# Performance work log

Measured on AMD Instinct MI355X. Metric: run time of the kernel, lower is better.

The kernel has to match this reference:

```python
import jax, jax.numpy as jnp
import numpy as np

B, T, W, H = 4, 4096, 1024, 8
BW = W // H  # block width


@jax.custom_vjp
def sqrt_bound(x):
    return jnp.sqrt(x)

def _sb_fwd(x):
    return jnp.sqrt(x), x

def _sb_bwd(x, g):
    return (g / jnp.sqrt(jnp.clip(4.0 * x, 1e-6)),)

sqrt_bound.defvjp(_sb_fwd, _sb_bwd)


def block_diag_linear(x, w, b):
    # x: [B,T,W] -> [B,T,H,BW]; w: [H,BW,BW]; b: [H,BW]
    xb = x.reshape(x.shape[0], x.shape[1], H, BW)
    y = jnp.einsum('bthi,hij->bthj', xb, w) + b
    return y.reshape(x.shape)


def setup_inputs() -> dict:
    key = jax.random.key(0)
    k1, k2, k3, k4 = jax.random.split(key, 4)
    x = jax.random.normal(k1, (B, T, W), dtype=jnp.float32)
    segment_pos = jnp.broadcast_to(jnp.arange(T, dtype=jnp.int32)[None, :], (B, T))
    std = 1.0 / np.sqrt(BW)
    w_in = std * jax.random.normal(k2, (H, BW, BW), dtype=jnp.float32)
    b_in = jnp.zeros((H, BW), dtype=jnp.float32)
    w_a = std * jax.random.normal(k3, (H, BW, BW), dtype=jnp.float32)
    b_a = jnp.zeros((H, BW), dtype=jnp.float32)
    # rnn_param_init: a_param = log(u^{-0.5} - 1), u ~ U(min_rad^2+eps, max_rad^2+eps)
    u = jax.random.uniform(k4, (W,), dtype=jnp.float32,
                           minval=0.9 ** 2 + 1e-8, maxval=0.999 ** 2 + 1e-8)
    a_param = jnp.log(jnp.exp(-0.5 * jnp.log(u)) - 1.0)
    return {'x': x, 'segment_pos': segment_pos, 'a_param': a_param,
            'w_in': w_in, 'b_in': b_in, 'w_a': w_a, 'b_a': b_a}


def reference(x, segment_pos, a_param, w_in, b_in, w_a, b_a):
    gate_x = jax.nn.sigmoid(block_diag_linear(x, w_in, b_in))
    gate_a = jax.nn.sigmoid(block_diag_linear(x, w_a, b_a))
    log_a = -8.0 * gate_a * jax.nn.softplus(a_param)  # [B,T,W]
    a = jnp.exp(log_a)
    multiplier = sqrt_bound(1.0 - jnp.exp(2.0 * log_a))
    normed_x = x * gate_x * multiplier
    reset = (segment_pos == 0)  # [B,T] bool
    a_eff = a * (~reset)[..., None].astype(a.dtype)
    # diagonal linear recurrence h_t = a_t * h_{t-1} + x_t via lax.scan over time
    def step(h, inp):
        a_t, x_t = inp
        h = a_t * h + x_t
        return h, h
    xs = (jnp.swapaxes(a_eff, 0, 1), jnp.swapaxes(normed_x, 0, 1))  # [T,B,W]
    h0 = jnp.zeros((x.shape[0], x.shape[2]), dtype=x.dtype)
    _, ys = jax.lax.scan(step, h0, xs)
    return jnp.swapaxes(ys, 0, 1)  # [B,T,W]
```

## Files before the change

### kernel.cpp

```cpp
#include <hip/hip_runtime.h>
#include <math.h>

#define NB 4
#define NT 4096
#define NW 1024
#define NH 8
#define CHUNK 64
#define NCH 64
#define STRIDE_A 136

typedef __attribute__((ext_vector_type(8))) short short8;
typedef __attribute__((ext_vector_type(4))) float f32x4;
typedef unsigned long long u64;

__device__ __forceinline__ short bf16rne(float f) {
    unsigned u = __float_as_uint(f);
    u += 0x7fffu + ((u >> 16) & 1u);
    return (short)(u >> 16);
}

__global__ __launch_bounds__(256)
void k0_wfrag(const float* __restrict__ w_in, const float* __restrict__ w_a,
              short* __restrict__ wfH, uint4* __restrict__ poison)
{
    int idx = blockIdx.x * 256 + threadIdx.x;
    uint4 nv; nv.x = nv.y = nv.z = nv.w = 0xFFFFFFFFu;
    poison[idx]         = nv;
    poison[idx + 65536] = nv;

    int j4 = (idx & 31) * 4;
    int i  = (idx >> 5) & 127;
    int h  = (idx >> 12) & 7;
    int g  = idx >> 15;
    const float* w = g ? w_a : w_in;
    float4 v = *(const float4*)&w[((size_t)h * 128 + i) * 128 + j4];
    const float vf[4] = {v.x, v.y, v.z, v.w};
    const int ks = i >> 5, q = (i >> 3) & 3, jj = i & 7;
    #pragma unroll
    for (int d = 0; d < 4; ++d) {
        int j = j4 + d;
        int lane = q * 16 + (j & 15);
        int ntg = j >> 4;
        size_t dst = ((size_t)(((h * 2 + g) * 4 + ks) * 8 + ntg) * 64 + lane) * 8 + jj;
        wfH[dst] = bf16rne(vf[d]);
    }
}

__global__ __launch_bounds__(512)
void k_fused(const float* __restrict__ x, const int* __restrict__ seg,
             const float* __restrict__ a_param,
             const float* __restrict__ b_in, const float* __restrict__ b_a,
             const short* __restrict__ wfH,
             float2* __restrict__ AGH, float* __restrict__ out)
{
    __shared__ short sA[CHUNK * STRIDE_A];
    __shared__ int   sSeg[CHUNK];

    const int h   = blockIdx.x;
    const int bc  = blockIdx.y;
    const int b   = bc >> 6, c = bc & 63;
    const int tid = threadIdx.x;
    const int wave = tid >> 6, lane = tid & 63;
    const int quad = lane >> 4, m = lane & 15;
    const int row0 = b * NT + c * CHUNK;

    {
        const int r  = tid >> 3;
        const int k0 = (tid & 7) * 16;
        const float4* px = (const float4*)(x + (size_t)(row0 + r) * NW + h * 128 + k0);
        float4 v0 = px[0], v1 = px[1], v2 = px[2], v3 = px[3];
        const float f[16] = {v0.x, v0.y, v0.z, v0.w, v1.x, v1.y, v1.z, v1.w,
                             v2.x, v2.y, v2.z, v2.w, v3.x, v3.y, v3.z, v3.w};
        short8 s0, s1;
        #pragma unroll
        for (int j = 0; j < 8; ++j) { s0[j] = bf16rne(f[j]); s1[j] = bf16rne(f[8 + j]); }
        *(short8*)&sA[r * STRIDE_A + k0]     = s0;
        *(short8*)&sA[r * STRIDE_A + k0 + 8] = s1;
        if ((tid & 7) == 0) sSeg[r] = seg[row0 + r];
    }
    __syncthreads();

    f32x4 acc[2][4];
    #pragma unroll
    for (int g = 0; g < 2; ++g)
        #pragma unroll
        for (int mt = 0; mt < 4; ++mt)
            acc[g][mt] = (f32x4){0.f, 0.f, 0.f, 0.f};

    #pragma unroll
    for (int ks = 0; ks < 4; ++ks) {
        short8 ah[4];
        #pragma unroll
        for (int mt = 0; mt < 4; ++mt)
            ah[mt] = *(const short8*)&sA[(mt * 16 + m) * STRIDE_A + ks * 32 + quad * 8];
        #pragma unroll
        for (int g = 0; g < 2; ++g) {
            const size_t fo = ((size_t)(((h * 2 + g) * 4 + ks) * 8 + wave) * 64 + lane) * 8;
            short8 bh = *(const short8*)(wfH + fo);
            #pragma unroll
            for (int mt = 0; mt < 4; ++mt)
                acc[g][mt] = __builtin_amdgcn_mfma_f32_16x16x32_bf16(ah[mt], bh, acc[g][mt], 0, 0, 0);
        }
    }

    const int col  = wave * 16 + m;
    const int colg = h * 128 + col;
    const float bi = b_in[colg];
    const float ba = b_a[colg];
    const float c2 = -8.0f * log1pf(expf(a_param[colg]));

    float cA = 1.f, cH = 0.f;
    float Pf[4][4], Hf[4][4];
    #pragma unroll
    for (int mt = 0; mt < 4; ++mt) {
        float lP[4], lH[4];
        {
            float xv[4];
            #pragma unroll
            for (int r = 0; r < 4; ++r) {
                const int rowi = row0 + mt * 16 + quad * 4 + r;
                xv[r] = x[(size_t)rowi * NW + colg];
            }
            const int4 sv4 = *(const int4*)&sSeg[mt * 16 + quad * 4];
            const int sv[4] = {sv4.x, sv4.y, sv4.z, sv4.w};
            #pragma unroll
            for (int r = 0; r < 4; ++r) {
                const float zx = acc[0][mt][r] + bi;
                const float za = acc[1][mt][r] + ba;
                const float gx = __fdividef(1.f, 1.f + __expf(-zx));
                const float ga = __fdividef(1.f, 1.f + __expf(-za));
                const float a  = __expf(c2 * ga);
                const float mult = sqrtf(fmaxf(fmaf(-a, a, 1.f), 0.f));
                const float av = (sv[r] == 0) ? 0.f : a;
                const float nx = xv[r] * gx * mult;
                lP[r] = (r == 0) ? av : lP[r - 1] * av;
                lH[r] = (r == 0) ? nx : fmaf(av, lH[r - 1], nx);
            }
        }
        float iA = lP[3], iH = lH[3];
        float uA = __shfl_up(iA, 16), uH = __shfl_up(iH, 16);
        if (quad >= 1) { iH = fmaf(iA, uH, iH); iA = uA * iA; }
        uA = __shfl_up(iA, 32); uH = __shfl_up(iH, 32);
        if (quad >= 2) { iH = fmaf(iA, uH, iH); iA = uA * iA; }
        float eA = __shfl_up(iA, 16), eH = __shfl_up(iH, 16);
        if (quad == 0) { eA = 1.f; eH = 0.f; }
        const float mAt = __shfl(iA, 48 + m);
        const float mHt = __shfl(iH, 48 + m);
        const float pA = cA * eA;
        const float pH = fmaf(eA, cH, eH);
        cH = fmaf(mAt, cH, mHt);
        cA = cA * mAt;
        #pragma unroll
        for (int r = 0; r < 4; ++r) {
            Pf[mt][r] = pA * lP[r];
            Hf[mt][r] = fmaf(lP[r], pH, lH[r]);
        }
    }

    const size_t cb0 = (size_t)(h * NB + b) * NCH * 128;
    if (quad == 0) {
        const u64 pk = ((u64)__float_as_uint(cH) << 32) | (u64)__float_as_uint(cA);
        __hip_atomic_store((u64*)&AGH[cb0 + (size_t)c * 128 + col], pk,
                           __ATOMIC_RELAXED, __HIP_MEMORY_SCOPE_AGENT);
    }

    float hp = 0.f;
    {
        float accA = 1.f;
        const int nw = (c + 15) >> 4;
        for (int w = 0; w < nw; ++w) {
            const int base = c - 1 - (w * 16 + quad * 4);
            const int nj   = base < 0 ? 0 : (base >= 3 ? 4 : base + 1);
            float a_ = 1.f, h_ = 0.f;
            if (nj > 0) {
                int folded = 0;
                for (;;) {
                    u64 pk[4];
                    #pragma unroll
                    for (int j = 0; j < 4; ++j) {
                        int idx = base - j; idx = idx < 0 ? 0 : idx;
                        pk[j] = __hip_atomic_load((const u64*)&AGH[cb0 + (size_t)idx * 128 + col],
                                                  __ATOMIC_RELAXED, __HIP_MEMORY_SCOPE_AGENT);
                    }
                    bool stall = false;
                    #pragma unroll
                    for (int j = 0; j < 4; ++j) {
                        if (j < folded || j >= nj || stall) continue;
                        const float A_ = __uint_as_float((unsigned)pk[j]);
                        if (__builtin_isnan(A_)) { stall = true; continue; }
                        const float H_ = __uint_as_float((unsigned)(pk[j] >> 32));
                        h_ = fmaf(a_, H_, h_);
                        a_ *= A_;
                        folded = j + 1;
                    }
                    if (folded >= nj) break;
                    __builtin_amdgcn_s_sleep(4);
                }
            }
            #pragma unroll
            for (int q = 0; q < 4; ++q) {
                const float Aq = __shfl(a_, q * 16 + m);
                const float Hq = __shfl(h_, q * 16 + m);
                hp = fmaf(accA, Hq, hp);
                accA *= Aq;
            }
        }
    }

    #pragma unroll
    for (int mt = 0; mt < 4; ++mt) {
        #pragma unroll
        for (int r = 0; r < 4; ++r) {
            const int rowi = row0 + mt * 16 + quad * 4 + r;
            out[(size_t)rowi * NW + colg] = fmaf(Pf[mt][r], hp, Hf[mt][r]);
        }
    }
}

extern "C" void kernel_launch(void* const* d_in, const int* in_sizes, int n_in,
                              void* d_out, int out_size, void* d_ws, size_t ws_size,
                              hipStream_t stream)
{
    (void)in_sizes; (void)n_in; (void)out_size; (void)ws_size;
    const float* x    = (const float*)d_in[0];
    const int*   seg  = (const int*)  d_in[1];
    const float* ap   = (const float*)d_in[2];
    const float* w_in = (const float*)d_in[3];
    const float* b_in = (const float*)d_in[4];
    const float* w_a  = (const float*)d_in[5];
    const float* b_a  = (const float*)d_in[6];
    float* out = (float*)d_out;

    const size_t NTOP = (size_t)NH * NB * NCH * 128;
    float2* AGH = (float2*)d_ws;
    short*  wfH = (short*)(AGH + NTOP);

    k0_wfrag<<<256, 256, 0, stream>>>(w_in, w_a, wfH, (uint4*)AGH);
    dim3 g1(NH, NB * NCH);
    k_fused<<<g1, 512, 0, stream>>>(x, seg, ap, b_in, b_a, wfH, AGH, out);
}
```

Before: 163.8 us.

## Process two batch chunks per block and use cheaper bf16/exp2 conversions

Each block now handles two batch rows (b and b+2) for the same chunk in a sequential loop, halving the grid to 1024 blocks. Per-column constants are hoisted out of that loop. The bf16 conversion now uses the packed v_cvt_pk_bf16_f32 instruction, sigmoid and exp use raw exp2 with log2e folding, the reset mask becomes a float multiply, and the sqrt clamp is removed. The goal is to cut instruction count and block launch overhead. The cost is less parallelism, and spin-waiting blocks now serialize two tasks, which raises the risk of stalls in the decoupled lookback.

```diff
diff --git a/kernel.cpp b/kernel.cpp
--- a/kernel.cpp
+++ b/kernel.cpp
@@ -8,6 +8,7 @@
 #define CHUNK 64
 #define NCH 64
 #define STRIDE_A 136
+#define LOG2E 1.4426950408889634f
 
 typedef __attribute__((ext_vector_type(8))) short short8;
 typedef __attribute__((ext_vector_type(4))) float f32x4;
@@ -17,6 +18,12 @@
     unsigned u = __float_as_uint(f);
     u += 0x7fffu + ((u >> 16) & 1u);
     return (short)(u >> 16);
+}
+
+__device__ __forceinline__ unsigned cvtpk(float lo, float hi) {
+    unsigned r;
+    asm("v_cvt_pk_bf16_f32 %0, %1, %2" : "=v"(r) : "v"(lo), "v"(hi));
+    return r;
 }
 
 __global__ __launch_bounds__(256)
@@ -54,165 +61,172 @@
              float2* __restrict__ AGH, float* __restrict__ out)
 {
     __shared__ short sA[CHUNK * STRIDE_A];
-    __shared__ int   sSeg[CHUNK];
+    __shared__ float sMask[CHUNK];
 
     const int h   = blockIdx.x;
-    const int bc  = blockIdx.y;
-    const int b   = bc >> 6, c = bc & 63;
+    const int bc2 = blockIdx.y;
+    const int bp  = bc2 >> 6, c = bc2 & 63;
     const int tid = threadIdx.x;
     const int wave = tid >> 6, lane = tid & 63;
     const int quad = lane >> 4, m = lane & 15;
-    const int row0 = b * NT + c * CHUNK;
-
-    {
-        const int r  = tid >> 3;
-        const int k0 = (tid & 7) * 16;
-        const float4* px = (const float4*)(x + (size_t)(row0 + r) * NW + h * 128 + k0);
-        float4 v0 = px[0], v1 = px[1], v2 = px[2], v3 = px[3];
-        const float f[16] = {v0.x, v0.y, v0.z, v0.w, v1.x, v1.y, v1.z, v1.w,
-                             v2.x, v2.y, v2.z, v2.w, v3.x, v3.y, v3.z, v3.w};
-        short8 s0, s1;
-        #pragma unroll
-        for (int j = 0; j < 8; ++j) { s0[j] = bf16rne(f[j]); s1[j] = bf16rne(f[8 + j]); }
-        *(short8*)&sA[r * STRIDE_A + k0]     = s0;
-        *(short8*)&sA[r * STRIDE_A + k0 + 8] = s1;
-        if ((tid & 7) == 0) sSeg[r] = seg[row0 + r];
-    }
-    __syncthreads();
-
-    f32x4 acc[2][4];
-    #pragma unroll
-    for (int g = 0; g < 2; ++g)
-        #pragma unroll
-        for (int mt = 0; mt < 4; ++mt)
-            acc[g][mt] = (f32x4){0.f, 0.f, 0.f, 0.f};
-
-    #pragma unroll
-    for (int ks = 0; ks < 4; ++ks) {
-        short8 ah[4];
-        #pragma unroll
-        for (int mt = 0; mt < 4; ++mt)
-            ah[mt] = *(const short8*)&sA[(mt * 16 + m) * STRIDE_A + ks * 32 + quad * 8];
-        #pragma unroll
-        for (int g = 0; g < 2; ++g) {
-            const size_t fo = ((size_t)(((h * 2 + g) * 4 + ks) * 8 + wave) * 64 + lane) * 8;
-            short8 bh = *(const short8*)(wfH + fo);
-            #pragma unroll
-            for (int mt = 0; mt < 4; ++mt)
-                acc[g][mt] = __builtin_amdgcn_mfma_f32_16x16x32_bf16(ah[mt], bh, acc[g][mt], 0, 0, 0);
-        }
-    }
 
     const int col  = wave * 16 + m;
     const int colg = h * 128 + col;
-    const float bi = b_in[colg];
-    const float ba = b_a[colg];
-    const float c2 = -8.0f * log1pf(expf(a_param[colg]));
-
-    float cA = 1.f, cH = 0.f;
-    float Pf[4][4], Hf[4][4];
-    #pragma unroll
-    for (int mt = 0; mt < 4; ++mt) {
-        float lP[4], lH[4];
+    const float bi2 = -LOG2E * b_in[colg];
+    const float ba2 = -LOG2E * b_a[colg];
+    const float c2l = -8.0f * LOG2E * log1pf(expf(a_param[colg]));
+
+    #pragma unroll 1
+    for (int task = 0; task < 2; ++task) {
+        const int b    = bp + task * 2;
+        const int row0 = b * NT + c * CHUNK;
+
+        if (task) __syncthreads();
+
         {
-            float xv[4];
+            const int r  = tid >> 3;
+            const int k0 = (tid & 7) * 16;
+            const float4* px = (const float4*)(x + (size_t)(row0 + r) * NW + h * 128 + k0);
+            float4 v0 = px[0], v1 = px[1], v2 = px[2], v3 = px[3];
+            uint4 u0, u1;
+            u0.x = cvtpk(v0.x, v0.y); u0.y = cvtpk(v0.z, v0.w);
+            u0.z = cvtpk(v1.x, v1.y); u0.w = cvtpk(v1.z, v1.w);
+            u1.x = cvtpk(v2.x, v2.y); u1.y = cvtpk(v2.z, v2.w);
+            u1.z = cvtpk(v3.x, v3.y); u1.w = cvtpk(v3.z, v3.w);
+            *(uint4*)&sA[r * STRIDE_A + k0]     = u0;
+            *(uint4*)&sA[r * STRIDE_A + k0 + 8] = u1;
+            if ((tid & 7) == 0) sMask[r] = (seg[row0 + r] == 0) ? 0.f : 1.f;
+        }
+        __syncthreads();
+
+        f32x4 acc[2][4];
+        #pragma unroll
+        for (int g = 0; g < 2; ++g)
+            #pragma unroll
+            for (int mt = 0; mt < 4; ++mt)
+                acc[g][mt] = (f32x4){0.f, 0.f, 0.f, 0.f};
+
+        #pragma unroll
+        for (int ks = 0; ks < 4; ++ks) {
+            short8 ah[4];
+            #pragma unroll
+            for (int mt = 0; mt < 4; ++mt)
+                ah[mt] = *(const short8*)&sA[(mt * 16 + m) * STRIDE_A + ks * 32 + quad * 8];
+            #pragma unroll
+            for (int g = 0; g < 2; ++g) {
+                const size_t fo = ((size_t)(((h * 2 + g) * 4 + ks) * 8 + wave) * 64 + lane) * 8;
+                short8 bh = *(const short8*)(wfH + fo);
+                #pragma unroll
+                for (int mt = 0; mt < 4; ++mt)
+                    acc[g][mt] = __builtin_amdgcn_mfma_f32_16x16x32_bf16(ah[mt], bh, acc[g][mt], 0, 0, 0);
+            }
+        }
+
+        float cA = 1.f, cH = 0.f;
+        float Pf[4][4], Hf[4][4];
+        #pragma unroll
+        for (int mt = 0; mt < 4; ++mt) {
+            float lP[4], lH[4];
+            {
+                float xv[4];
+                #pragma unroll
+                for (int r = 0; r < 4; ++r) {
+                    const int rowi = row0 + mt * 16 + quad * 4 + r;
+                    xv[r] = x[(size_t)rowi * NW + colg];
+                }
+                const float4 mk4 = *(const float4*)&sMask[mt * 16 + quad * 4];
+                const float mk[4] = {mk4.x, mk4.y, mk4.z, mk4.w};
+                #pragma unroll
+                for (int r = 0; r < 4; ++r) {
+                    const float ex = __builtin_amdgcn_exp2f(fmaf(acc[0][mt][r], -LOG2E, bi2));
+                    const float gx = __fdividef(1.f, 1.f + ex);
+                    const float ea = __builtin_amdgcn_exp2f(fmaf(acc[1][mt][r], -LOG2E, ba2));
+                    const float ga = __fdividef(1.f, 1.f + ea);
+                    const float a  = __builtin_amdgcn_exp2f(c2l * ga);
+                    const float mult = __builtin_amdgcn_sqrtf(fmaf(-a, a, 1.f));
+                    const float av = a * mk[r];
+                    const float nx = xv[r] * gx * mult;
+                    lP[r] = (r == 0) ? av : lP[r - 1] * av;
+                    lH[r] = (r == 0) ? nx : fmaf(av, lH[r - 1], nx);
+                }
+            }
+            float iA = lP[3], iH = lH[3];
+            float uA = __shfl_up(iA, 16), uH = __shfl_up(iH, 16);
+            if (quad >= 1) { iH = fmaf(iA, uH, iH); iA = uA * iA; }
+            uA = __shfl_up(iA, 32); uH = __shfl_up(iH, 32);
+            if (quad >= 2) { iH = fmaf(iA, uH, iH); iA = uA * iA; }
+            float eA = __shfl_up(iA, 16), eH = __shfl_up(iH, 16);
+            if (quad == 0) { eA = 1.f; eH = 0.f; }
+            const float mAt = __shfl(iA, 48 + m);
+            const float mHt = __shfl(iH, 48 + m);
+            const float pA = cA * eA;
+            const float pH = fmaf(eA, cH, eH);
+            cH = fmaf(mAt, cH, mHt);
+            cA = cA * mAt;
+            #pragma unroll
+            for (int r = 0; r < 4; ++r) {
+                Pf[mt][r] = pA * lP[r];
+                Hf[mt][r] = fmaf(lP[r], pH, lH[r]);
+            }
+        }
+
+        const size_t cb0 = (size_t)(h * NB + b) * NCH * 128;
+        if (quad == 0) {
+            const u64 pk = ((u64)__float_as_uint(cH) << 32) | (u64)__float_as_uint(cA);
+            __hip_atomic_store((u64*)&AGH[cb0 + (size_t)c * 128 + col], pk,
+                               __ATOMIC_RELAXED, __HIP_MEMORY_SCOPE_AGENT);
+        }
+
+        float hp = 0.f;
+        {
+            float accA = 1.f;
+            const int nw = (c + 15) >> 4;
+            for (int w = 0; w < nw; ++w) {
+                const int base = c - 1 - (w * 16 + quad * 4);
+                const int nj   = base < 0 ? 0 : (base >= 3 ? 4 : base + 1);
+                float a_ = 1.f, h_ = 0.f;
+                if (nj > 0) {
+                    int folded = 0;
+                    for (;;) {
+                        u64 pk[4];
+                        #pragma unroll
+                        for (int j = 0; j < 4; ++j) {
+                            int idx = base - j; idx = idx < 0 ? 0 : idx;
+                            pk[j] = __hip_atomic_load((const u64*)&AGH[cb0 + (size_t)idx * 128 + col],
+                                                      __ATOMIC_RELAXED, __HIP_MEMORY_SCOPE_AGENT);
+                        }
+                        bool stall = false;
+                        #pragma unroll
+                        for (int j = 0; j < 4; ++j) {
+                            if (j < folded || j >= nj || stall) continue;
+                            const float A_ = __uint_as_float((unsigned)pk[j]);
+                            if (__builtin_isnan(A_)) { stall = true; continue; }
+                            const float H_ = __uint_as_float((unsigned)(pk[j] >> 32));
+                            h_ = fmaf(a_, H_, h_);
+                            a_ *= A_;
+                            folded = j + 1;
+                        }
+                        if (folded >= nj) break;
+                        __builtin_amdgcn_s_sleep(4);
+                    }
+                }
+                #pragma unroll
+                for (int q = 0; q < 4; ++q) {
+                    const float Aq = __shfl(a_, q * 16 + m);
+                    const float Hq = __shfl(h_, q * 16 + m);
+                    hp = fmaf(accA, Hq, hp);
+                    accA *= Aq;
+                }
+            }
+        }
+
+        #pragma unroll
+        for (int mt = 0; mt < 4; ++mt) {
             #pragma unroll
             for (int r = 0; r < 4; ++r) {
                 const int rowi = row0 + mt * 16 + quad * 4 + r;
-                xv[r] = x[(size_t)rowi * NW + colg];
-            }
-            const int4 sv4 = *(const int4*)&sSeg[mt * 16 + quad * 4];
-            const int sv[4] = {sv4.x, sv4.y, sv4.z, sv4.w};
-            #pragma unroll
-            for (int r = 0; r < 4; ++r) {
-                const float zx = acc[0][mt][r] + bi;
-                const float za = acc[1][mt][r] + ba;
-                const float gx = __fdividef(1.f, 1.f + __expf(-zx));
-                const float ga = __fdividef(1.f, 1.f + __expf(-za));
-                const float a  = __expf(c2 * ga);
-                const float mult = sqrtf(fmaxf(fmaf(-a, a, 1.f), 0.f));
-                const float av = (sv[r] == 0) ? 0.f : a;
-                const float nx = xv[r] * gx * mult;
-                lP[r] = (r == 0) ? av : lP[r - 1] * av;
-                lH[r] = (r == 0) ? nx : fmaf(av, lH[r - 1], nx);
-            }
-        }
-        float iA = lP[3], iH = lH[3];
-        float uA = __shfl_up(iA, 16), uH = __shfl_up(iH, 16);
-        if (quad >= 1) { iH = fmaf(iA, uH, iH); iA = uA * iA; }
-        uA = __shfl_up(iA, 32); uH = __shfl_up(iH, 32);
-        if (quad >= 2) { iH = fmaf(iA, uH, iH); iA = uA * iA; }
-        float eA = __shfl_up(iA, 16), eH = __shfl_up(iH, 16);
-        if (quad == 0) { eA = 1.f; eH = 0.f; }
-        const float mAt = __shfl(iA, 48 + m);
-        const float mHt = __shfl(iH, 48 + m);
-        const float pA = cA * eA;
-        const float pH = fmaf(eA, cH, eH);
-        cH = fmaf(mAt, cH, mHt);
-        cA = cA * mAt;
-        #pragma unroll
-        for (int r = 0; r < 4; ++r) {
-            Pf[mt][r] = pA * lP[r];
-            Hf[mt][r] = fmaf(lP[r], pH, lH[r]);
-        }
-    }
-
-    const size_t cb0 = (size_t)(h * NB + b) * NCH * 128;
-    if (quad == 0) {
-        const u64 pk = ((u64)__float_as_uint(cH) << 32) | (u64)__float_as_uint(cA);
-        __hip_atomic_store((u64*)&AGH[cb0 + (size_t)c * 128 + col], pk,
-                           __ATOMIC_RELAXED, __HIP_MEMORY_SCOPE_AGENT);
-    }
-
-    float hp = 0.f;
-    {
-        float accA = 1.f;
-        const int nw = (c + 15) >> 4;
-        for (int w = 0; w < nw; ++w) {
-            const int base = c - 1 - (w * 16 + quad * 4);
-            const int nj   = base < 0 ? 0 : (base >= 3 ? 4 : base + 1);
-            float a_ = 1.f, h_ = 0.f;
-            if (nj > 0) {
-                int folded = 0;
-                for (;;) {
-                    u64 pk[4];
-                    #pragma unroll
-                    for (int j = 0; j < 4; ++j) {
-                        int idx = base - j; idx = idx < 0 ? 0 : idx;
-                        pk[j] = __hip_atomic_load((const u64*)&AGH[cb0 + (size_t)idx * 128 + col],
-                                                  __ATOMIC_RELAXED, __HIP_MEMORY_SCOPE_AGENT);
-                    }
-                    bool stall = false;
-                    #pragma unroll
-                    for (int j = 0; j < 4; ++j) {
-                        if (j < folded || j >= nj || stall) continue;
-                        const float A_ = __uint_as_float((unsigned)pk[j]);
-                        if (__builtin_isnan(A_)) { stall = true; continue; }
-                        const float H_ = __uint_as_float((unsigned)(pk[j] >> 32));
-                        h_ = fmaf(a_, H_, h_);
-                        a_ *= A_;
-                        folded = j + 1;
-                    }
-                    if (folded >= nj) break;
-                    __builtin_amdgcn_s_sleep(4);
-                }
-            }
-            #pragma unroll
-            for (int q = 0; q < 4; ++q) {
-                const float Aq = __shfl(a_, q * 16 + m);
-                const float Hq = __shfl(h_, q * 16 + m);
-                hp = fmaf(accA, Hq, hp);
-                accA *= Aq;
-            }
-        }
-    }
-
-    #pragma unroll
-    for (int mt = 0; mt < 4; ++mt) {
-        #pragma unroll
-        for (int r = 0; r < 4; ++r) {
-            const int rowi = row0 + mt * 16 + quad * 4 + r;
-            out[(size_t)rowi * NW + colg] = fmaf(Pf[mt][r], hp, Hf[mt][r]);
+                out[(size_t)rowi * NW + colg] = fmaf(Pf[mt][r], hp, Hf[mt][r]);
+            }
         }
     }
 }
@@ -236,6 +250,6 @@
     short*  wfH = (short*)(AGH + NTOP);
 
     k0_wfrag<<<256, 256, 0, stream>>>(w_in, w_a, wfH, (uint4*)AGH);
-    dim3 g1(NH, NB * NCH);
+    dim3 g1(NH, 128);
     k_fused<<<g1, 512, 0, stream>>>(x, seg, ap, b_in, b_a, wfH, AGH, out);
 }
```

Result: slower. 168.6 us (+3.0%).
